# Kernel optimization log

Hardware: AMD Instinct MI355X
Metric: run time of the kernel (lower is better)

Reference implementation:

```python
import jax, jax.numpy as jnp
import numpy as np

B, L, V, D, H, DK, NL, M = 4, 1024, 64, 256, 4, 64, 4, 20
FF = 4 * D
EPS = 1e-5


def _rel_table(seq_len, m):
    # abs(i-j), log-bucketed beyond m, clipped to [0, 2m] -> int indices [L, L]
    d = jnp.abs(jnp.arange(seq_len)[:, None] - jnp.arange(seq_len)[None, :]).astype(jnp.float32)
    d = jnp.where(d > m, m + jnp.log2(jnp.maximum(d - m, 1.0)), d)
    return jnp.clip(d, 0, 2 * m).astype(jnp.int32)


def _layer_norm(x, g, b):
    mu = jnp.mean(x, axis=-1, keepdims=True)
    var = jnp.mean(jnp.square(x - mu), axis=-1, keepdims=True)
    return (x - mu) * jax.lax.rsqrt(var + EPS) * g + b


def setup_inputs() -> dict:
    key = jax.random.key(0)
    ks = jax.random.split(key, 16)
    w = lambda i, shape: jax.random.normal(ks[i], shape, jnp.float32) * 0.05
    return {
        "x": jax.random.normal(ks[0], (B, L, V), jnp.float32),
        "emb": w(1, (V, D)),
        "Wq": w(2, (NL, D, H * DK)), "bq": jnp.zeros((NL, H * DK), jnp.float32),
        "Wk": w(3, (NL, D, H * DK)), "bk": jnp.zeros((NL, H * DK), jnp.float32),
        "Wv": w(4, (NL, D, H * DK)), "bv": jnp.zeros((NL, H * DK), jnp.float32),
        "Wo": w(5, (NL, H * DK, D)), "bo": jnp.zeros((NL, D), jnp.float32),
        "rel_k": 1.0 + w(6, (NL, 2 * M + 1, H)),  # multiplicative bias ~1
        "rel_b": w(7, (NL, 2 * M + 1, H)),
        "ln1_g": jnp.ones((NL, D), jnp.float32), "ln1_b": jnp.zeros((NL, D), jnp.float32),
        "W1": w(8, (NL, D, FF)), "b1": jnp.zeros((NL, FF), jnp.float32),
        "W2": w(9, (NL, FF, D)), "b2": jnp.zeros((NL, D), jnp.float32),
        "ln2_g": jnp.ones((NL, D), jnp.float32), "ln2_b": jnp.zeros((NL, D), jnp.float32),
    }


def reference(x, emb, Wq, bq, Wk, bk, Wv, bv, Wo, bo, rel_k, rel_b,
              ln1_g, ln1_b, W1, b1, W2, b2, ln2_g, ln2_b):
    h = x @ emb  # [B, L, D]  (dropout inactive: eval mode)
    table = _rel_table(L, M)  # [L, L] int32
    inv_sqrt_dk = jnp.float32(1.0 / np.sqrt(DK))
    attns = []
    for l in range(NL):
        q = (h @ Wq[l] + bq[l]).reshape(B, L, H, DK)
        k = (h @ Wk[l] + bk[l]).reshape(B, L, H, DK)
        v = (h @ Wv[l] + bv[l]).reshape(B, L, H, DK)
        scores = jnp.einsum('blhk,bmhk->bhlm', q, k) * inv_sqrt_dk
        # per-head relative-position bias (table symmetric, so axis order of L,L is immaterial)
        bias_k = jnp.transpose(rel_k[l][table], (2, 1, 0))  # [H, L, L]
        bias_b = jnp.transpose(rel_b[l][table], (2, 1, 0))  # [H, L, L]
        scores = scores * bias_k[None] + bias_b[None]
        attn = jax.nn.softmax(scores, axis=-1)  # attn dropout inactive (eval)
        attns.append(attn)
        out = jnp.einsum('bhlm,bmhk->blhk', attn, v).reshape(B, L, H * DK) @ Wo[l] + bo[l]
        # FeedForwardNetwork (note: source has NO residual connections)
        y = _layer_norm(out, ln1_g[l], ln1_b[l])
        y = jax.nn.gelu(y @ W1[l] + b1[l], approximate=False) @ W2[l] + b2[l]
        h = _layer_norm(y, ln2_g[l], ln2_b[l])
    avg_attn = jnp.mean(jnp.stack(attns, axis=0), axis=0)  # [B, H, L, L]
    return h.mean(axis=1), avg_attn
```

## Files before the change

### kernel.cpp

```cpp
#include <hip/hip_runtime.h>
#include <hip/hip_bf16.h>
#include <math.h>

#define Bn 4
#define Ln 1024
#define Vn 64
#define Dn 256
#define Hn 4
#define DKn 64
#define NLn 4
#define Mn 20
#define FFn 1024
#define NTOK (Bn * Ln)
#define QKVW 768
#define LOG2E 1.4426950408889634f
#define PELEMS (Bn * Hn * Ln * Ln)

typedef __attribute__((ext_vector_type(8))) short bf16x8;
typedef __attribute__((ext_vector_type(4))) float f32x4;

__device__ __forceinline__ ushort f2b(float f) {
    uint u = __float_as_uint(f);
    u += 0x7fff + ((u >> 16) & 1);
    return (ushort)(u >> 16);
}
__device__ __forceinline__ float b2f(ushort u) {
    return __uint_as_float(((uint)u) << 16);
}

__global__ __launch_bounds__(256) void embed_k(const float* __restrict__ X,
                                               const float* __restrict__ E,
                                               ushort* __restrict__ Hb) {
    __shared__ float xs[Vn];
    int n = blockIdx.x, d = threadIdx.x;
    if (threadIdx.x < Vn) xs[threadIdx.x] = X[n * Vn + threadIdx.x];
    __syncthreads();
    float s = 0.f;
#pragma unroll
    for (int v = 0; v < Vn; ++v) s += xs[v] * E[v * Dn + d];
    Hb[(size_t)n * Dn + d] = f2b(s);
}

__global__ __launch_bounds__(256) void relbias_k(const float* __restrict__ rk,
                                                 const float* __restrict__ rb,
                                                 float* __restrict__ bkT,
                                                 float* __restrict__ bbT) {
    int tid = blockIdx.x * 256 + threadIdx.x;
    int dist = tid & 1023;
    int hh = (tid >> 10) & 3;
    int l = tid >> 12;
    float dd = (float)dist;
    if (dist > Mn) dd = (float)Mn + log2f((float)(dist - Mn));
    if (dd > 2.0f * Mn) dd = 2.0f * Mn;
    int idx = (int)dd;
    bkT[tid] = rk[(l * (2 * Mn + 1) + idx) * Hn + hh] * 0.125f * LOG2E;
    bbT[tid] = rb[(l * (2 * Mn + 1) + idx) * Hn + hh] * LOG2E;
}

__global__ __launch_bounds__(256) void prep_bias(const float* __restrict__ bq,
                                                 const float* __restrict__ bk,
                                                 const float* __restrict__ bv,
                                                 float* __restrict__ bqkv) {
    int idx = blockIdx.x * 256 + threadIdx.x;
    int l = idx / QKVW, r = idx - l * QKVW;
    float v;
    if (r < 256)      v = bq[l * 256 + r];
    else if (r < 512) v = bk[l * 256 + r - 256];
    else              v = bv[l * 256 + r - 512];
    bqkv[idx] = v;
}

__global__ __launch_bounds__(256) void transpose_cvt(
    const float* __restrict__ src, ushort* __restrict__ dst,
    int R, int C, int srcLS, int dstLS) {
    __shared__ float s[32][33];
    src += (size_t)blockIdx.z * srcLS;
    dst += (size_t)blockIdx.z * dstLS;
    int r0 = blockIdx.y * 32, c0 = blockIdx.x * 32;
    int tx = threadIdx.x & 31, ty = threadIdx.x >> 5;
#pragma unroll
    for (int ii = 0; ii < 4; ++ii)
        s[ty + 8 * ii][tx] = src[(size_t)(r0 + ty + 8 * ii) * C + c0 + tx];
    __syncthreads();
#pragma unroll
    for (int ii = 0; ii < 4; ++ii)
        dst[(size_t)(c0 + ty + 8 * ii) * R + r0 + tx] = f2b(s[tx][ty + 8 * ii]);
}

__global__ __launch_bounds__(256) void transpose_v(const ushort* __restrict__ qkv,
                                                   ushort* __restrict__ Vt) {
    __shared__ ushort s[32][65];
    int j0 = blockIdx.x * 32;
    int bh = blockIdx.y;
    int b = bh >> 2, hh = bh & 3;
    int t = threadIdx.x;
#pragma unroll
    for (int ii = 0; ii < 8; ++ii) {
        int e = t + 256 * ii;
        int jr = e >> 6, dc = e & 63;
        s[jr][dc] = qkv[(size_t)(b * Ln + j0 + jr) * QKVW + 2 * Dn + hh * DKn + dc];
    }
    __syncthreads();
#pragma unroll
    for (int ii = 0; ii < 8; ++ii) {
        int e = t + 256 * ii;
        int dr = e >> 5, jc = e & 31;
        Vt[(size_t)(bh * DKn + dr) * Ln + j0 + jc] = s[jc][dr];
    }
}

#define GST 40
__global__ __launch_bounds__(256) void gemm_mfma(
    const ushort* __restrict__ A, const ushort* __restrict__ Bt,
    const float* __restrict__ bias, ushort* __restrict__ C,
    int M, int N, int K, int act) {
    __shared__ __align__(16) ushort As[64 * GST];
    __shared__ __align__(16) ushort Bs[64 * GST];
    int t = threadIdx.x;
    int lane = t & 63, w = t >> 6;
    int wm = w >> 1, wn = w & 1;
    int l15 = lane & 15, lg = lane >> 4;
    int mBase = blockIdx.y * 64, nBase = blockIdx.x * 64;
    int lrow = t >> 2, lkc = (t & 3) * 8;
    const ushort* Ap = A + (size_t)(mBase + lrow) * K + lkc;
    const ushort* Bp = Bt + (size_t)(nBase + lrow) * K + lkc;
    f32x4 acc[2][2] = {};
    for (int k0 = 0; k0 < K; k0 += 32) {
        uint4 av = *(const uint4*)(Ap + k0);
        uint4 bv = *(const uint4*)(Bp + k0);
        __syncthreads();
        *(uint4*)&As[lrow * GST + lkc] = av;
        *(uint4*)&Bs[lrow * GST + lkc] = bv;
        __syncthreads();
        bf16x8 a0 = *(const bf16x8*)&As[(wm * 32 + l15) * GST + lg * 8];
        bf16x8 a1 = *(const bf16x8*)&As[(wm * 32 + 16 + l15) * GST + lg * 8];
        bf16x8 b0 = *(const bf16x8*)&Bs[(wn * 32 + l15) * GST + lg * 8];
        bf16x8 b1 = *(const bf16x8*)&Bs[(wn * 32 + 16 + l15) * GST + lg * 8];
        acc[0][0] = __builtin_amdgcn_mfma_f32_16x16x32_bf16(a0, b0, acc[0][0], 0, 0, 0);
        acc[0][1] = __builtin_amdgcn_mfma_f32_16x16x32_bf16(a0, b1, acc[0][1], 0, 0, 0);
        acc[1][0] = __builtin_amdgcn_mfma_f32_16x16x32_bf16(a1, b0, acc[1][0], 0, 0, 0);
        acc[1][1] = __builtin_amdgcn_mfma_f32_16x16x32_bf16(a1, b1, acc[1][1], 0, 0, 0);
    }
#pragma unroll
    for (int ni = 0; ni < 2; ++ni) {
        int col = nBase + wn * 32 + ni * 16 + l15;
        float bc = bias[col];
#pragma unroll
        for (int mi = 0; mi < 2; ++mi) {
            int rb = mBase + wm * 32 + mi * 16 + lg * 4;
#pragma unroll
            for (int j = 0; j < 4; ++j) {
                float v = acc[mi][ni][j] + bc;
                if (act) v = v * 0.5f * (1.0f + erff(v * 0.7071067811865475f));
                C[(size_t)(rb + j) * N + col] = f2b(v);
            }
        }
    }
}

#define PWST 40
#define NW 8
template <int MODE>
__global__ __launch_bounds__(512) void attn_fused(
    const ushort* __restrict__ qkv, const ushort* __restrict__ Vt,
    const float* __restrict__ bkTab, const float* __restrict__ bbTab,
    ushort* __restrict__ ctx, float* __restrict__ avg,
    ushort* __restrict__ Pout, int first) {
    __shared__ float bk_l[Ln];
    __shared__ float bb_l[Ln];
    __shared__ __align__(16) ushort Pw[NW][2][16 * PWST];
    __shared__ float mm[NW][16];
    __shared__ float ll[NW][16];
    __shared__ float Opart[NW][1024];

    int t = threadIdx.x;
    int lane = t & 63, w = t >> 6;
    int wn = w & 3, wc = w >> 2;
    int l15 = lane & 15, lg = lane >> 4;

    int bid = blockIdx.x;
    int xcd = bid & 7, sub = bid >> 3;
    int bh = xcd * 2 + (sub >> 6);
    int q = sub & 63;
    int b = bh >> 2, hh = bh & 3;
    int i0 = q * 16;

#pragma unroll
    for (int ii = 0; ii < 2; ++ii) {
        bk_l[t + 512 * ii] = bkTab[hh * Ln + t + 512 * ii];
        bb_l[t + 512 * ii] = bbTab[hh * Ln + t + 512 * ii];
    }
    __syncthreads();

    bf16x8 qa0, qa1;
    {
        const ushort* qp = qkv + (size_t)(b * Ln + i0 + l15) * QKVW + hh * DKn;
        qa0 = *(const bf16x8*)(qp + lg * 8);
        qa1 = *(const bf16x8*)(qp + 32 + lg * 8);
    }

    const ushort* kbase = qkv + (size_t)(b * Ln) * QKVW + Dn + hh * DKn;

    f32x4 sv[8];
    float m[4] = {-1e30f, -1e30f, -1e30f, -1e30f};
#pragma unroll
    for (int cl = 0; cl < 8; ++cl) {
        int c = wc * 8 + cl;
        const ushort* kp = kbase + (size_t)(c * 64 + wn * 16 + l15) * QKVW;
        bf16x8 k0 = *(const bf16x8*)(kp + lg * 8);
        bf16x8 k1 = *(const bf16x8*)(kp + 32 + lg * 8);
        f32x4 acc = {};
        acc = __builtin_amdgcn_mfma_f32_16x16x32_bf16(qa0, k0, acc, 0, 0, 0);
        acc = __builtin_amdgcn_mfma_f32_16x16x32_bf16(qa1, k1, acc, 0, 0, 0);
        int j = c * 64 + wn * 16 + l15;
#pragma unroll
        for (int r = 0; r < 4; ++r) {
            int i = i0 + lg * 4 + r;
            int dist = (i > j) ? (i - j) : (j - i);
            float s = acc[r] * bk_l[dist] + bb_l[dist];
            sv[cl][r] = s;
            m[r] = fmaxf(m[r], s);
        }
    }
#pragma unroll
    for (int mask = 1; mask < 16; mask <<= 1)
#pragma unroll
        for (int r = 0; r < 4; ++r) m[r] = fmaxf(m[r], __shfl_xor(m[r], mask, 64));
    if (l15 == 0)
#pragma unroll
        for (int r = 0; r < 4; ++r) mm[w][lg * 4 + r] = m[r];
    __syncthreads();
#pragma unroll
    for (int r = 0; r < 4; ++r) {
        int row = lg * 4 + r;
        float m0 = fmaxf(fmaxf(mm[0][row], mm[1][row]), fmaxf(mm[2][row], mm[3][row]));
        float m1 = fmaxf(fmaxf(mm[4][row], mm[5][row]), fmaxf(mm[6][row], mm[7][row]));
        m[r] = fmaxf(m0, m1);
    }
    float lsum[4] = {0.f, 0.f, 0.f, 0.f};
#pragma unroll
    for (int cl = 0; cl < 8; ++cl)
#pragma unroll
        for (int r = 0; r < 4; ++r) {
            float p = exp2f(sv[cl][r] - m[r]);
            sv[cl][r] = p;
            lsum[r] += p;
        }
#pragma unroll
    for (int mask = 1; mask < 16; mask <<= 1)
#pragma unroll
        for (int r = 0; r < 4; ++r) lsum[r] += __shfl_xor(lsum[r], mask, 64);
    if (l15 == 0)
#pragma unroll
        for (int r = 0; r < 4; ++r) ll[w][lg * 4 + r] = lsum[r];
    __syncthreads();
    float invl[4];
#pragma unroll
    for (int r = 0; r < 4; ++r) {
        int row = lg * 4 + r;
        invl[r] = 1.0f / (ll[0][row] + ll[1][row] + ll[2][row] + ll[3][row] +
                          ll[4][row] + ll[5][row] + ll[6][row] + ll[7][row]);
    }

    const ushort* vbase = Vt + (size_t)bh * DKn * Ln;
    float* avgrow = avg + ((size_t)bh * Ln + i0) * Ln;
    ushort* prow = Pout + ((size_t)bh * Ln + i0) * Ln;
    int iw = lane >> 2, jq = lane & 3;
    f32x4 acco[4] = {};
#pragma unroll
    for (int p = 0; p < 4; ++p) {
        const int c0 = wc * 8 + 2 * p, c1 = c0 + 1;
        float aold[2][4];
        if (MODE == 0 && !first) {
#pragma unroll
            for (int cc = 0; cc < 2; ++cc)
#pragma unroll
                for (int r = 0; r < 4; ++r)
                    aold[cc][r] = avgrow[(size_t)(lg * 4 + r) * Ln +
                                         (c0 + cc) * 64 + wn * 16 + l15];
        }
#pragma unroll
        for (int cc = 0; cc < 2; ++cc)
#pragma unroll
            for (int r = 0; r < 4; ++r) {
                float pv = sv[2 * p + cc][r] * invl[r];
                sv[2 * p + cc][r] = pv;
                ushort ph = f2b(pv);
                int off = (lg * 4 + r) * PWST + cc * 16 + l15;
                Pw[w][0][off] = ph;
                Pw[w][1][off] = f2b(pv - b2f(ph));
            }
        int kcol = (lg < 2 ? c0 : c1) * 64 + wn * 16 + (lg & 1) * 8;
        bf16x8 va0 = *(const bf16x8*)(vbase + (size_t)(0 * 16 + l15) * Ln + kcol);
        bf16x8 va1 = *(const bf16x8*)(vbase + (size_t)(1 * 16 + l15) * Ln + kcol);
        bf16x8 va2 = *(const bf16x8*)(vbase + (size_t)(2 * 16 + l15) * Ln + kcol);
        bf16x8 va3 = *(const bf16x8*)(vbase + (size_t)(3 * 16 + l15) * Ln + kcol);
        bf16x8 pbh = *(const bf16x8*)&Pw[w][0][l15 * PWST + lg * 8];
        bf16x8 pbl = *(const bf16x8*)&Pw[w][1][l15 * PWST + lg * 8];
        acco[0] = __builtin_amdgcn_mfma_f32_16x16x32_bf16(va0, pbh, acco[0], 0, 0, 0);
        acco[1] = __builtin_amdgcn_mfma_f32_16x16x32_bf16(va1, pbh, acco[1], 0, 0, 0);
        acco[2] = __builtin_amdgcn_mfma_f32_16x16x32_bf16(va2, pbh, acco[2], 0, 0, 0);
        acco[3] = __builtin_amdgcn_mfma_f32_16x16x32_bf16(va3, pbh, acco[3], 0, 0, 0);
        acco[0] = __builtin_amdgcn_mfma_f32_16x16x32_bf16(va0, pbl, acco[0], 0, 0, 0);
        acco[1] = __builtin_amdgcn_mfma_f32_16x16x32_bf16(va1, pbl, acco[1], 0, 0, 0);
        acco[2] = __builtin_amdgcn_mfma_f32_16x16x32_bf16(va2, pbl, acco[2], 0, 0, 0);
        acco[3] = __builtin_amdgcn_mfma_f32_16x16x32_bf16(va3, pbl, acco[3], 0, 0, 0);
        if (MODE == 0) {
#pragma unroll
            for (int cc = 0; cc < 2; ++cc)
#pragma unroll
                for (int r = 0; r < 4; ++r) {
                    float v = 0.25f * sv[2 * p + cc][r];
                    if (!first) v += aold[cc][r];
                    avgrow[(size_t)(lg * 4 + r) * Ln + (c0 + cc) * 64 + wn * 16 + l15] = v;
                }
        } else {
            ushort4 ph0 = *(const ushort4*)&Pw[w][0][iw * PWST + 0 * 16 + jq * 4];
            ushort4 ph1 = *(const ushort4*)&Pw[w][0][iw * PWST + 1 * 16 + jq * 4];
            *(ushort4*)&prow[(size_t)iw * Ln + c0 * 64 + wn * 16 + jq * 4] = ph0;
            *(ushort4*)&prow[(size_t)iw * Ln + c1 * 64 + wn * 16 + jq * 4] = ph1;
        }
    }

#pragma unroll
    for (int dg = 0; dg < 4; ++dg)
#pragma unroll
        for (int r = 0; r < 4; ++r)
            Opart[w][(dg * 16 + lg * 4 + r) * 16 + l15] = acco[dg][r];
    __syncthreads();
#pragma unroll
    for (int k = 0; k < 2; ++k) {
        int idx = t + 512 * k;
        float v = Opart[0][idx] + Opart[1][idx] + Opart[2][idx] + Opart[3][idx] +
                  Opart[4][idx] + Opart[5][idx] + Opart[6][idx] + Opart[7][idx];
        int dd = idx >> 4, ii = idx & 15;
        ctx[(size_t)(b * Ln + i0 + ii) * Dn + hh * DKn + dd] = f2b(v);
    }
}

__global__ __launch_bounds__(256) void avg_sum_k(const ushort* __restrict__ P,
                                                 float* __restrict__ avg) {
    size_t e = ((size_t)blockIdx.x * 256 + threadIdx.x) * 8;
    uint4 a = *(const uint4*)&P[e];
    uint4 b4 = *(const uint4*)&P[(size_t)PELEMS + e];
    uint4 c4 = *(const uint4*)&P[(size_t)2 * PELEMS + e];
    uint4 d4 = *(const uint4*)&P[(size_t)3 * PELEMS + e];
    const ushort* ap = (const ushort*)&a;
    const ushort* bp = (const ushort*)&b4;
    const ushort* cp = (const ushort*)&c4;
    const ushort* dp = (const ushort*)&d4;
    float4 o0, o1;
    float* o0p = (float*)&o0;
    float* o1p = (float*)&o1;
#pragma unroll
    for (int k = 0; k < 4; ++k)
        o0p[k] = 0.25f * (b2f(ap[k]) + b2f(bp[k]) + b2f(cp[k]) + b2f(dp[k]));
#pragma unroll
    for (int k = 0; k < 4; ++k)
        o1p[k] = 0.25f * (b2f(ap[4 + k]) + b2f(bp[4 + k]) + b2f(cp[4 + k]) + b2f(dp[4 + k]));
    *(float4*)&avg[e] = o0;
    *(float4*)&avg[e + 4] = o1;
}

__global__ __launch_bounds__(256) void layernorm_k(const ushort* __restrict__ X,
                                                   const float* __restrict__ g,
                                                   const float* __restrict__ bta,
                                                   ushort* __restrict__ Y) {
    int w = threadIdx.x >> 6, lane = threadIdx.x & 63;
    int row = blockIdx.x * 4 + w;
    const ushort* xr = X + (size_t)row * Dn;
    float x[4];
#pragma unroll
    for (int ii = 0; ii < 4; ++ii) x[ii] = b2f(xr[lane + 64 * ii]);
    float s = x[0] + x[1] + x[2] + x[3];
#pragma unroll
    for (int m = 1; m < 64; m <<= 1) s += __shfl_xor(s, m, 64);
    float mu = s * (1.0f / 256.0f);
    float vs = 0.f;
#pragma unroll
    for (int ii = 0; ii < 4; ++ii) {
        float d = x[ii] - mu;
        vs += d * d;
    }
#pragma unroll
    for (int m = 1; m < 64; m <<= 1) vs += __shfl_xor(vs, m, 64);
    float rs = rsqrtf(vs * (1.0f / 256.0f) + 1e-5f);
#pragma unroll
    for (int ii = 0; ii < 4; ++ii) {
        int d = lane + 64 * ii;
        Y[(size_t)row * Dn + d] = f2b((x[ii] - mu) * rs * g[d] + bta[d]);
    }
}

__global__ __launch_bounds__(256) void mean_part_k(const ushort* __restrict__ Hb,
                                                   float* __restrict__ part) {
    int blk = blockIdx.x;
    int b = blk >> 4, g = blk & 15;
    int d = threadIdx.x;
    float s = 0.f;
#pragma unroll
    for (int r = 0; r < 64; ++r)
        s += b2f(Hb[(size_t)(b * Ln + g * 64 + r) * Dn + d]);
    part[(size_t)blk * Dn + d] = s;
}
__global__ __launch_bounds__(256) void mean_final_k(const float* __restrict__ part,
                                                    float* __restrict__ out) {
    int b = blockIdx.x, d = threadIdx.x;
    float s = 0.f;
#pragma unroll
    for (int g = 0; g < 16; ++g) s += part[(size_t)(b * 16 + g) * Dn + d];
    out[b * Dn + d] = s * (1.0f / (float)Ln);
}

extern "C" void kernel_launch(void* const* d_in, const int* in_sizes, int n_in,
                              void* d_out, int out_size, void* d_ws, size_t ws_size,
                              hipStream_t stream) {
    const float* x    = (const float*)d_in[0];
    const float* emb  = (const float*)d_in[1];
    const float* Wq   = (const float*)d_in[2];
    const float* bq   = (const float*)d_in[3];
    const float* Wk   = (const float*)d_in[4];
    const float* bk   = (const float*)d_in[5];
    const float* Wv   = (const float*)d_in[6];
    const float* bv   = (const float*)d_in[7];
    const float* Wo   = (const float*)d_in[8];
    const float* bo   = (const float*)d_in[9];
    const float* rk   = (const float*)d_in[10];
    const float* rb   = (const float*)d_in[11];
    const float* ln1g = (const float*)d_in[12];
    const float* ln1b = (const float*)d_in[13];
    const float* W1   = (const float*)d_in[14];
    const float* b1   = (const float*)d_in[15];
    const float* W2   = (const float*)d_in[16];
    const float* b2   = (const float*)d_in[17];
    const float* ln2g = (const float*)d_in[18];
    const float* ln2b = (const float*)d_in[19];

    float* out = (float*)d_out;
    float* avg = out + Bn * Dn;

    char* ws = (char*)d_ws;
    const size_t MB = 1024 * 1024;
    ushort* hb   = (ushort*)(ws);
    ushort* qkvb = (ushort*)(ws + 2 * MB);
    ushort* ctxb = (ushort*)(ws + 8 * MB);
    ushort* t1   = (ushort*)(ws + 10 * MB);
    ushort* ffb  = (ushort*)(ws + 12 * MB);
    ushort* qkvT = (ushort*)(ws + 20 * MB);
    ushort* WoT  = (ushort*)(ws + 22 * MB);
    ushort* W1T  = (ushort*)(ws + 23 * MB);
    ushort* W2T  = (ushort*)(ws + 25 * MB);
    float*  bqkv = (float*)(ws + 27 * MB);
    float*  bkT  = (float*)(ws + 27 * MB + 65536);
    float*  bbT  = (float*)(ws + 27 * MB + 131072);
    ushort* Vt   = (ushort*)(ws + 30 * MB);
    float*  mpart= (float*)(ws + 33 * MB);
    ushort* Pbuf = (ushort*)(ws + 36 * MB);

    const size_t need = 36 * MB + (size_t)4 * PELEMS * sizeof(ushort);
    const bool fancy = (ws_size >= need);

    embed_k<<<NTOK, 256, 0, stream>>>(x, emb, hb);
    relbias_k<<<64, 256, 0, stream>>>(rk, rb, bkT, bbT);
    prep_bias<<<12, 256, 0, stream>>>(bq, bk, bv, bqkv);

    dim3 t88(8, 8, NLn);
    transpose_cvt<<<t88, 256, 0, stream>>>(Wq, qkvT + 0,      256, 256, 65536, 196608);
    transpose_cvt<<<t88, 256, 0, stream>>>(Wk, qkvT + 65536,  256, 256, 65536, 196608);
    transpose_cvt<<<t88, 256, 0, stream>>>(Wv, qkvT + 131072, 256, 256, 65536, 196608);
    transpose_cvt<<<t88, 256, 0, stream>>>(Wo, WoT,           256, 256, 65536, 65536);
    transpose_cvt<<<dim3(32, 8, NLn), 256, 0, stream>>>(W1, W1T, 256, 1024, 262144, 262144);
    transpose_cvt<<<dim3(8, 32, NLn), 256, 0, stream>>>(W2, W2T, 1024, 256, 262144, 262144);

    for (int l = 0; l < NLn; ++l) {
        gemm_mfma<<<dim3(12, 64), 256, 0, stream>>>(
            hb, qkvT + (size_t)l * 196608, bqkv + l * QKVW, qkvb, NTOK, QKVW, Dn, 0);
        transpose_v<<<dim3(32, 16), 256, 0, stream>>>(qkvb, Vt);
        if (fancy) {
            attn_fused<1><<<1024, 512, 0, stream>>>(
                qkvb, Vt, bkT + l * Hn * Ln, bbT + l * Hn * Ln, ctxb, avg,
                Pbuf + (size_t)l * PELEMS, (l == 0) ? 1 : 0);
        } else {
            attn_fused<0><<<1024, 512, 0, stream>>>(
                qkvb, Vt, bkT + l * Hn * Ln, bbT + l * Hn * Ln, ctxb, avg,
                (ushort*)Pbuf, (l == 0) ? 1 : 0);
        }
        gemm_mfma<<<dim3(4, 64), 256, 0, stream>>>(
            ctxb, WoT + (size_t)l * 65536, bo + l * 256, t1, NTOK, Dn, Dn, 0);
        layernorm_k<<<NTOK / 4, 256, 0, stream>>>(
            t1, ln1g + l * 256, ln1b + l * 256, t1);
        gemm_mfma<<<dim3(16, 64), 256, 0, stream>>>(
            t1, W1T + (size_t)l * 262144, b1 + l * FFn, ffb, NTOK, FFn, Dn, 1);
        gemm_mfma<<<dim3(4, 64), 256, 0, stream>>>(
            ffb, W2T + (size_t)l * 262144, b2 + l * 256, hb, NTOK, Dn, FFn, 0);
        layernorm_k<<<NTOK / 4, 256, 0, stream>>>(
            hb, ln2g + l * 256, ln2b + l * 256, hb);
    }
    if (fancy) {
        avg_sum_k<<<PELEMS / (256 * 8), 256, 0, stream>>>(Pbuf, avg);
    }
    mean_part_k<<<64, 256, 0, stream>>>(hb, mpart);
    mean_final_k<<<Bn, 256, 0, stream>>>(mpart, out);
}
```

Baseline: 419.3 us.

## Fuse layernorms into following GEMM A-tile loads and share attention LDS buffers

Removes the standalone layernorm kernels by computing row mean/variance inside the consuming GEMM (each row's 256 elements are held in registers across 4 threads) and normalizing while staging the A tile into shared memory. The final ln2 is applied once after the loop. It also overlays the attention kernel's P staging buffer and output partial-sum buffer in one per-wave LDS region to cut shared memory use. Each of the 12-16 N-blocks recomputes row statistics redundantly, and the fully unrolled K loop increases register pressure.

```diff
diff --git a/kernel.cpp b/kernel.cpp
--- a/kernel.cpp
+++ b/kernel.cpp
@@ -110,12 +110,26 @@
 }
 
 #define GST 40
+#define GEMM_FRAG_MFMA                                                        \
+    bf16x8 a0 = *(const bf16x8*)&As[(wm * 32 + l15) * GST + lg * 8];          \
+    bf16x8 a1 = *(const bf16x8*)&As[(wm * 32 + 16 + l15) * GST + lg * 8];     \
+    bf16x8 b0 = *(const bf16x8*)&Bs[(wn * 32 + l15) * GST + lg * 8];          \
+    bf16x8 b1 = *(const bf16x8*)&Bs[(wn * 32 + 16 + l15) * GST + lg * 8];     \
+    acc[0][0] = __builtin_amdgcn_mfma_f32_16x16x32_bf16(a0, b0, acc[0][0], 0, 0, 0); \
+    acc[0][1] = __builtin_amdgcn_mfma_f32_16x16x32_bf16(a0, b1, acc[0][1], 0, 0, 0); \
+    acc[1][0] = __builtin_amdgcn_mfma_f32_16x16x32_bf16(a1, b0, acc[1][0], 0, 0, 0); \
+    acc[1][1] = __builtin_amdgcn_mfma_f32_16x16x32_bf16(a1, b1, acc[1][1], 0, 0, 0);
+
+template <int LNA>
 __global__ __launch_bounds__(256) void gemm_mfma(
     const ushort* __restrict__ A, const ushort* __restrict__ Bt,
     const float* __restrict__ bias, ushort* __restrict__ C,
-    int M, int N, int K, int act) {
+    int M, int N, int K, int act,
+    const float* __restrict__ lng, const float* __restrict__ lnb) {
     __shared__ __align__(16) ushort As[64 * GST];
     __shared__ __align__(16) ushort Bs[64 * GST];
+    __shared__ float gl[256];
+    __shared__ float bl[256];
     int t = threadIdx.x;
     int lane = t & 63, w = t >> 6;
     int wm = w >> 1, wn = w & 1;
@@ -125,21 +139,64 @@
     const ushort* Ap = A + (size_t)(mBase + lrow) * K + lkc;
     const ushort* Bp = Bt + (size_t)(nBase + lrow) * K + lkc;
     f32x4 acc[2][2] = {};
-    for (int k0 = 0; k0 < K; k0 += 32) {
-        uint4 av = *(const uint4*)(Ap + k0);
-        uint4 bv = *(const uint4*)(Bp + k0);
+
+    if constexpr (LNA) {
+        uint4 areg[8];
+        float s = 0.f;
+#pragma unroll
+        for (int kc = 0; kc < 8; ++kc) {
+            areg[kc] = *(const uint4*)(Ap + kc * 32);
+            const ushort* e = (const ushort*)&areg[kc];
+#pragma unroll
+            for (int q = 0; q < 8; ++q) s += b2f(e[q]);
+        }
+        s += __shfl_xor(s, 1, 64);
+        s += __shfl_xor(s, 2, 64);
+        float mu = s * (1.0f / 256.0f);
+        float vv = 0.f;
+#pragma unroll
+        for (int kc = 0; kc < 8; ++kc) {
+            const ushort* e = (const ushort*)&areg[kc];
+#pragma unroll
+            for (int q = 0; q < 8; ++q) {
+                float d = b2f(e[q]) - mu;
+                vv += d * d;
+            }
+        }
+        vv += __shfl_xor(vv, 1, 64);
+        vv += __shfl_xor(vv, 2, 64);
+        float rs = rsqrtf(vv * (1.0f / 256.0f) + 1e-5f);
+        gl[t] = lng[t];
+        bl[t] = lnb[t];
         __syncthreads();
-        *(uint4*)&As[lrow * GST + lkc] = av;
-        *(uint4*)&Bs[lrow * GST + lkc] = bv;
-        __syncthreads();
-        bf16x8 a0 = *(const bf16x8*)&As[(wm * 32 + l15) * GST + lg * 8];
-        bf16x8 a1 = *(const bf16x8*)&As[(wm * 32 + 16 + l15) * GST + lg * 8];
-        bf16x8 b0 = *(const bf16x8*)&Bs[(wn * 32 + l15) * GST + lg * 8];
-        bf16x8 b1 = *(const bf16x8*)&Bs[(wn * 32 + 16 + l15) * GST + lg * 8];
-        acc[0][0] = __builtin_amdgcn_mfma_f32_16x16x32_bf16(a0, b0, acc[0][0], 0, 0, 0);
-        acc[0][1] = __builtin_amdgcn_mfma_f32_16x16x32_bf16(a0, b1, acc[0][1], 0, 0, 0);
-        acc[1][0] = __builtin_amdgcn_mfma_f32_16x16x32_bf16(a1, b0, acc[1][0], 0, 0, 0);
-        acc[1][1] = __builtin_amdgcn_mfma_f32_16x16x32_bf16(a1, b1, acc[1][1], 0, 0, 0);
+#pragma unroll
+        for (int kc = 0; kc < 8; ++kc) {
+            uint4 bv = *(const uint4*)(Bp + kc * 32);
+            __syncthreads();
+            {
+                const ushort* e = (const ushort*)&areg[kc];
+                ushort outv[8];
+#pragma unroll
+                for (int q = 0; q < 8; ++q) {
+                    int col = kc * 32 + lkc + q;
+                    outv[q] = f2b((b2f(e[q]) - mu) * rs * gl[col] + bl[col]);
+                }
+                *(uint4*)&As[lrow * GST + lkc] = *(const uint4*)outv;
+            }
+            *(uint4*)&Bs[lrow * GST + lkc] = bv;
+            __syncthreads();
+            GEMM_FRAG_MFMA
+        }
+    } else {
+        for (int k0 = 0; k0 < K; k0 += 32) {
+            uint4 av = *(const uint4*)(Ap + k0);
+            uint4 bv = *(const uint4*)(Bp + k0);
+            __syncthreads();
+            *(uint4*)&As[lrow * GST + lkc] = av;
+            *(uint4*)&Bs[lrow * GST + lkc] = bv;
+            __syncthreads();
+            GEMM_FRAG_MFMA
+        }
     }
 #pragma unroll
     for (int ni = 0; ni < 2; ++ni) {
@@ -168,15 +225,17 @@
     ushort* __restrict__ Pout, int first) {
     __shared__ float bk_l[Ln];
     __shared__ float bb_l[Ln];
-    __shared__ __align__(16) ushort Pw[NW][2][16 * PWST];
+    __shared__ __align__(16) char uni[NW][4096];
     __shared__ float mm[NW][16];
     __shared__ float ll[NW][16];
-    __shared__ float Opart[NW][1024];
 
     int t = threadIdx.x;
     int lane = t & 63, w = t >> 6;
     int wn = w & 3, wc = w >> 2;
     int l15 = lane & 15, lg = lane >> 4;
+
+    ushort* pwh = (ushort*)&uni[w][0];
+    ushort* pwl = (ushort*)&uni[w][1280];
 
     int bid = blockIdx.x;
     int xcd = bid & 7, sub = bid >> 3;
@@ -287,16 +346,16 @@
                 sv[2 * p + cc][r] = pv;
                 ushort ph = f2b(pv);
                 int off = (lg * 4 + r) * PWST + cc * 16 + l15;
-                Pw[w][0][off] = ph;
-                Pw[w][1][off] = f2b(pv - b2f(ph));
+                pwh[off] = ph;
+                pwl[off] = f2b(pv - b2f(ph));
             }
         int kcol = (lg < 2 ? c0 : c1) * 64 + wn * 16 + (lg & 1) * 8;
         bf16x8 va0 = *(const bf16x8*)(vbase + (size_t)(0 * 16 + l15) * Ln + kcol);
         bf16x8 va1 = *(const bf16x8*)(vbase + (size_t)(1 * 16 + l15) * Ln + kcol);
         bf16x8 va2 = *(const bf16x8*)(vbase + (size_t)(2 * 16 + l15) * Ln + kcol);
         bf16x8 va3 = *(const bf16x8*)(vbase + (size_t)(3 * 16 + l15) * Ln + kcol);
-        bf16x8 pbh = *(const bf16x8*)&Pw[w][0][l15 * PWST + lg * 8];
-        bf16x8 pbl = *(const bf16x8*)&Pw[w][1][l15 * PWST + lg * 8];
+        bf16x8 pbh = *(const bf16x8*)&pwh[l15 * PWST + lg * 8];
+        bf16x8 pbl = *(const bf16x8*)&pwl[l15 * PWST + lg * 8];
         acco[0] = __builtin_amdgcn_mfma_f32_16x16x32_bf16(va0, pbh, acco[0], 0, 0, 0);
         acco[1] = __builtin_amdgcn_mfma_f32_16x16x32_bf16(va1, pbh, acco[1], 0, 0, 0);
         acco[2] = __builtin_amdgcn_mfma_f32_16x16x32_bf16(va2, pbh, acco[2], 0, 0, 0);
@@ -315,24 +374,28 @@
                     avgrow[(size_t)(lg * 4 + r) * Ln + (c0 + cc) * 64 + wn * 16 + l15] = v;
                 }
         } else {
-            ushort4 ph0 = *(const ushort4*)&Pw[w][0][iw * PWST + 0 * 16 + jq * 4];
-            ushort4 ph1 = *(const ushort4*)&Pw[w][0][iw * PWST + 1 * 16 + jq * 4];
+            ushort4 ph0 = *(const ushort4*)&pwh[iw * PWST + 0 * 16 + jq * 4];
+            ushort4 ph1 = *(const ushort4*)&pwh[iw * PWST + 1 * 16 + jq * 4];
             *(ushort4*)&prow[(size_t)iw * Ln + c0 * 64 + wn * 16 + jq * 4] = ph0;
             *(ushort4*)&prow[(size_t)iw * Ln + c1 * 64 + wn * 16 + jq * 4] = ph1;
         }
     }
 
-#pragma unroll
-    for (int dg = 0; dg < 4; ++dg)
-#pragma unroll
-        for (int r = 0; r < 4; ++r)
-            Opart[w][(dg * 16 + lg * 4 + r) * 16 + l15] = acco[dg][r];
+    {
+        float* op = (float*)&uni[w][0];
+#pragma unroll
+        for (int dg = 0; dg < 4; ++dg)
+#pragma unroll
+            for (int r = 0; r < 4; ++r)
+                op[(dg * 16 + lg * 4 + r) * 16 + l15] = acco[dg][r];
+    }
     __syncthreads();
 #pragma unroll
     for (int k = 0; k < 2; ++k) {
         int idx = t + 512 * k;
-        float v = Opart[0][idx] + Opart[1][idx] + Opart[2][idx] + Opart[3][idx] +
-                  Opart[4][idx] + Opart[5][idx] + Opart[6][idx] + Opart[7][idx];
+        float v = 0.f;
+#pragma unroll
+        for (int wv = 0; wv < NW; ++wv) v += ((const float*)&uni[wv][0])[idx];
         int dd = idx >> 4, ii = idx & 15;
         ctx[(size_t)(b * Ln + i0 + ii) * Dn + hh * DKn + dd] = f2b(v);
     }
@@ -473,8 +536,15 @@
     transpose_cvt<<<dim3(8, 32, NLn), 256, 0, stream>>>(W2, W2T, 1024, 256, 262144, 262144);
 
     for (int l = 0; l < NLn; ++l) {
-        gemm_mfma<<<dim3(12, 64), 256, 0, stream>>>(
-            hb, qkvT + (size_t)l * 196608, bqkv + l * QKVW, qkvb, NTOK, QKVW, Dn, 0);
+        if (l == 0) {
+            gemm_mfma<0><<<dim3(12, 64), 256, 0, stream>>>(
+                hb, qkvT + (size_t)l * 196608, bqkv + l * QKVW, qkvb,
+                NTOK, QKVW, Dn, 0, nullptr, nullptr);
+        } else {
+            gemm_mfma<1><<<dim3(12, 64), 256, 0, stream>>>(
+                hb, qkvT + (size_t)l * 196608, bqkv + l * QKVW, qkvb,
+                NTOK, QKVW, Dn, 0, ln2g + (l - 1) * 256, ln2b + (l - 1) * 256);
+        }
         transpose_v<<<dim3(32, 16), 256, 0, stream>>>(qkvb, Vt);
         if (fancy) {
             attn_fused<1><<<1024, 512, 0, stream>>>(
@@ -485,17 +555,18 @@
                 qkvb, Vt, bkT + l * Hn * Ln, bbT + l * Hn * Ln, ctxb, avg,
                 (ushort*)Pbuf, (l == 0) ? 1 : 0);
         }
-        gemm_mfma<<<dim3(4, 64), 256, 0, stream>>>(
-            ctxb, WoT + (size_t)l * 65536, bo + l * 256, t1, NTOK, Dn, Dn, 0);
-        layernorm_k<<<NTOK / 4, 256, 0, stream>>>(
-            t1, ln1g + l * 256, ln1b + l * 256, t1);
-        gemm_mfma<<<dim3(16, 64), 256, 0, stream>>>(
-            t1, W1T + (size_t)l * 262144, b1 + l * FFn, ffb, NTOK, FFn, Dn, 1);
-        gemm_mfma<<<dim3(4, 64), 256, 0, stream>>>(
-            ffb, W2T + (size_t)l * 262144, b2 + l * 256, hb, NTOK, Dn, FFn, 0);
-        layernorm_k<<<NTOK / 4, 256, 0, stream>>>(
-            hb, ln2g + l * 256, ln2b + l * 256, hb);
-    }
+        gemm_mfma<0><<<dim3(4, 64), 256, 0, stream>>>(
+            ctxb, WoT + (size_t)l * 65536, bo + l * 256, t1,
+            NTOK, Dn, Dn, 0, nullptr, nullptr);
+        gemm_mfma<1><<<dim3(16, 64), 256, 0, stream>>>(
+            t1, W1T + (size_t)l * 262144, b1 + l * FFn, ffb,
+            NTOK, FFn, Dn, 1, ln1g + l * 256, ln1b + l * 256);
+        gemm_mfma<0><<<dim3(4, 64), 256, 0, stream>>>(
+            ffb, W2T + (size_t)l * 262144, b2 + l * 256, hb,
+            NTOK, Dn, FFn, 0, nullptr, nullptr);
+    }
+    layernorm_k<<<NTOK / 4, 256, 0, stream>>>(
+        hb, ln2g + 3 * 256, ln2b + 3 * 256, hb);
     if (fancy) {
         avg_sum_k<<<PELEMS / (256 * 8), 256, 0, stream>>>(Pbuf, avg);
     }
```

Result: no change. 416.1 us (-0.8%).
